# Performance work log

Measured on AMD Instinct MI355X. Metric: run time of the kernel, lower is better.

## Reference

```python
import jax, jax.numpy as jnp
import numpy as np

B, H, W = 32, 56, 56
C_IN, C_OUT, GROUPS, K = 256, 256, 32, 3
EPS = 1e-5


def setup_inputs() -> dict:
    key = jax.random.key(0)
    k1, k2 = jax.random.split(key, 2)
    x = jax.random.normal(k1, (B, H, W, C_IN), dtype=jnp.float32)
    # HWIO grouped-conv kernel: I = C_IN // GROUPS = 8; equivalent to the
    # concatenation of the 32 per-group [3,3,8,8] Conv2d kernels along O.
    w = jax.random.normal(k2, (K, K, C_IN // GROUPS, C_OUT), dtype=jnp.float32) * 0.05
    b = jnp.zeros((C_OUT,), dtype=jnp.float32)
    gamma = jnp.ones((C_OUT,), dtype=jnp.float32)
    beta = jnp.zeros((C_OUT,), dtype=jnp.float32)
    return {"x": x, "w": w, "b": b, "gamma": gamma, "beta": beta}


def reference(x, w, b, gamma, beta):
    # Grouped conv: same math as tf.split -> per-group Conv2d -> tf.concat,
    # expressed as one native grouped convolution (feature_group_count).
    y = jax.lax.conv_general_dilated(
        x, w,
        window_strides=(1, 1),
        padding="SAME",
        dimension_numbers=("NHWC", "HWIO", "NHWC"),
        feature_group_count=GROUPS,
    ) + b  # [B,H,W,C_OUT]
    # BatchNorm (training forward: batch statistics over N,H,W per channel)
    mean = jnp.mean(y, axis=(0, 1, 2))
    var = jnp.var(y, axis=(0, 1, 2))
    y = (y - mean) * jax.lax.rsqrt(var + EPS) * gamma + beta
    # Act('relu')
    return jax.nn.relu(y)
```

## Files before the change

kernel.cpp:

```cpp
#include <hip/hip_runtime.h>
#include <hip/hip_bf16.h>

#define BB 32
#define HH 56
#define WW 56
#define CC 256
#define NPIX (BB*HH*WW)
#define GRP 32
#define GSZ (NPIX*8)
#define EPS 1e-5f

typedef short bf16x8 __attribute__((ext_vector_type(8)));
typedef float f32x4  __attribute__((ext_vector_type(4)));

__device__ __forceinline__ unsigned short f2bf(float f) {
    __hip_bfloat16 h = __float2bfloat16(f);
    return *reinterpret_cast<unsigned short*>(&h);
}


__global__ void k0_zero(float* stats) { stats[threadIdx.x] = 0.f; }

__global__ __launch_bounds__(256) void k_pre(
    const float* __restrict__ x, __hip_bfloat16* __restrict__ xg)
{
    __shared__ unsigned short lx[32*260];
    const int t  = threadIdx.x;
    const int P0 = blockIdx.x * 32;

    #pragma unroll
    for (int r = 0; r < 8; ++r) {
        const int id  = r*256 + t;
        const int pix = id >> 6;
        const int c4  = id & 63;
        float4 v = *(const float4*)(x + (size_t)(P0+pix)*CC + c4*4);
        ushort4 s;
        s.x = f2bf(v.x); s.y = f2bf(v.y); s.z = f2bf(v.z); s.w = f2bf(v.w);
        *(ushort4*)(lx + pix*260 + c4*4) = s;
    }
    __syncthreads();
    #pragma unroll
    for (int r = 0; r < 4; ++r) {
        const int oid = r*256 + t;
        const int pl  = oid & 31;
        const int g   = oid >> 5;
        ushort4 a = *(const ushort4*)(lx + pl*260 + g*8);
        ushort4 c = *(const ushort4*)(lx + pl*260 + g*8 + 4);
        __hip_bfloat16* dst = xg + (size_t)g*GSZ + (size_t)(P0+pl)*8;
        *(ushort4*)dst       = a;
        *(ushort4*)(dst + 4) = c;
    }
}

__global__ __launch_bounds__(256, 5) void k1_conv(
    const __hip_bfloat16* __restrict__ xg, const float* __restrict__ wgt,
    __hip_bfloat16* __restrict__ y, float* __restrict__ stats)
{
    __shared__ unsigned short xt[10*58*24];
    __shared__ float bsum[16], bsq[16];

    const int gp = blockIdx.x;
    const int hb = blockIdx.y;
    const int b  = blockIdx.z;
    const int t  = threadIdx.x;
    const int h0 = hb * 8;

    if (t < 16) { bsum[t] = 0.f; bsq[t] = 0.f; }

    #pragma unroll
    for (int j = 0; j < 5; ++j) {
        const int e   = j*256 + t;
        const int col = e % 58;
        const int rg  = e / 58;
        const int row = rg >> 1;
        const int g   = rg & 1;
        const int hh  = h0 - 1 + row;
        const int wc  = col - 1;
        uint4 v = make_uint4(0u, 0u, 0u, 0u);
        if (e < 1160 && (unsigned)hh < HH && (unsigned)wc < WW)
            v = *(const uint4*)(xg + (size_t)(gp*2+g)*GSZ
                                   + (size_t)((b*HH + hh)*WW + wc)*8);
        if (e < 1160)
            *(uint4*)(xt + (row*58 + col)*24 + g*8) = v;
    }

    const int lane = t & 63;
    const int rp   = t >> 6;
    const int n    = lane & 15;
    const int q    = lane >> 4;

    bf16x8 wfrag[5];
    #pragma unroll
    for (int s = 0; s < 5; ++s) {
        const int o   = s*4 + q;
        const int g   = (o >= 10);
        const int tap = o - g*10;
        bf16x8 f = {0,0,0,0,0,0,0,0};
        if (tap < 9 && (n >> 3) == g) {
            #pragma unroll
            for (int e = 0; e < 8; ++e)
                f[e] = (short)f2bf(wgt[(tap*8 + e)*CC + gp*16 + n]);
        }
        wfrag[s] = f;
    }

    __syncthreads();

    const int m    = lane & 15;
    const int rowr = rp*2 + (m >> 3);
    const int colb = m & 7;

    int aoff[5];
    #pragma unroll
    for (int s = 0; s < 5; ++s) {
        int o  = s*4 + q;
        int g  = (o >= 10);
        int tp = o - g*10;
        if (tp == 9) tp = 0;
        int dh = tp / 3, dw = tp - dh*3;
        aoff[s] = ((rowr + dh)*58 + colb + dw)*24 + g*8;
    }

    const int h = h0 + rowr;
    const size_t pixbase = ((size_t)(b*HH + h))*WW;
    float lsum[4] = {0.f, 0.f, 0.f, 0.f};
    float lsq[4]  = {0.f, 0.f, 0.f, 0.f};

    #pragma unroll 2
    for (int ct = 0; ct < 7; ++ct) {
        f32x4 acc = {0.f, 0.f, 0.f, 0.f};
        #pragma unroll
        for (int s = 0; s < 5; ++s) {
            bf16x8 af = *(const bf16x8*)(xt + aoff[s] + ct*192);
            acc = __builtin_amdgcn_mfma_f32_16x16x32_bf16(wfrag[s], af, acc, 0, 0, 0);
        }
        ushort4 st;
        st.x = f2bf(acc[0]); st.y = f2bf(acc[1]);
        st.z = f2bf(acc[2]); st.w = f2bf(acc[3]);
        *(ushort4*)(y + (pixbase + ct*8 + colb)*CC + gp*16 + q*4) = st;
        #pragma unroll
        for (int i = 0; i < 4; ++i) {
            lsum[i] += acc[i];
            lsq[i]  += acc[i]*acc[i];
        }
    }

    #pragma unroll
    for (int d = 8; d >= 1; d >>= 1) {
        #pragma unroll
        for (int i = 0; i < 4; ++i) {
            lsum[i] += __shfl_xor(lsum[i], d);
            lsq[i]  += __shfl_xor(lsq[i],  d);
        }
    }
    if (m == 0) {
        #pragma unroll
        for (int i = 0; i < 4; ++i) {
            atomicAdd(&bsum[q*4 + i], lsum[i]);
            atomicAdd(&bsq[q*4 + i],  lsq[i]);
        }
    }
    __syncthreads();
    if (t < 16) {
        atomicAdd(&stats[gp*16 + t],       bsum[t]);
        atomicAdd(&stats[256 + gp*16 + t], bsq[t]);
    }
}

__global__ void k2_finalize(const float* __restrict__ stats,
                            const float* __restrict__ gamma,
                            const float* __restrict__ beta,
                            float* __restrict__ ss)
{
    int c = threadIdx.x;
    float inv_n = 1.f / (float)NPIX;
    float mean = stats[c] * inv_n;
    float var  = stats[256 + c] * inv_n - mean * mean;
    float scale = gamma[c] * rsqrtf(var + EPS);
    ss[c]       = scale;
    ss[256 + c] = beta[c] - mean * scale;
}

__global__ __launch_bounds__(256) void k3_norm(
    const __hip_bfloat16* __restrict__ y, const float* __restrict__ ss,
    float* __restrict__ out)
{
    const int t   = threadIdx.x;
    const int oct = t & 31;
    const int pr  = t >> 5;
    const int c0  = oct * 8;

    float4 sc0 = *(const float4*)(ss + c0);
    float4 sc1 = *(const float4*)(ss + c0 + 4);
    float4 sh0 = *(const float4*)(ss + 256 + c0);
    float4 sh1 = *(const float4*)(ss + 256 + c0 + 4);

    const uint4* yv = (const uint4*)y;
    float4* ov = (float4*)out;
    const int px0 = blockIdx.x * 32 + pr;

    uint4 d[4];
    #pragma unroll
    for (int i = 0; i < 4; ++i)
        d[i] = yv[(size_t)(px0 + i*8)*32 + oct];

    #pragma unroll
    for (int i = 0; i < 4; ++i) {
        const int px = px0 + i*8;
        float f0 = __uint_as_float((d[i].x & 0xffffu) << 16);
        float f1 = __uint_as_float(d[i].x & 0xffff0000u);
        float f2 = __uint_as_float((d[i].y & 0xffffu) << 16);
        float f3 = __uint_as_float(d[i].y & 0xffff0000u);
        float f4 = __uint_as_float((d[i].z & 0xffffu) << 16);
        float f5 = __uint_as_float(d[i].z & 0xffff0000u);
        float f6 = __uint_as_float((d[i].w & 0xffffu) << 16);
        float f7 = __uint_as_float(d[i].w & 0xffff0000u);

        float4 o0, o1;
        o0.x = fmaxf(0.f, f0 * sc0.x + sh0.x);
        o0.y = fmaxf(0.f, f1 * sc0.y + sh0.y);
        o0.z = fmaxf(0.f, f2 * sc0.z + sh0.z);
        o0.w = fmaxf(0.f, f3 * sc0.w + sh0.w);
        o1.x = fmaxf(0.f, f4 * sc1.x + sh1.x);
        o1.y = fmaxf(0.f, f5 * sc1.y + sh1.y);
        o1.z = fmaxf(0.f, f6 * sc1.z + sh1.z);
        o1.w = fmaxf(0.f, f7 * sc1.w + sh1.w);

        ov[(size_t)px*64 + oct*2]     = o0;
        ov[(size_t)px*64 + oct*2 + 1] = o1;
    }
}

extern "C" void kernel_launch(void* const* d_in, const int* in_sizes, int n_in,
                              void* d_out, int out_size, void* d_ws, size_t ws_size,
                              hipStream_t stream) {
    const float* x     = (const float*)d_in[0];
    const float* wgt   = (const float*)d_in[1];
    const float* gamma = (const float*)d_in[3];
    const float* beta  = (const float*)d_in[4];
    float* out = (float*)d_out;

    float* stats = (float*)d_ws;
    float* ss    = (float*)((char*)d_ws + 2048);
    __hip_bfloat16* y  = (__hip_bfloat16*)((char*)d_ws + 4096);
    __hip_bfloat16* xg = (__hip_bfloat16*)((char*)d_ws + 4096 + (size_t)NPIX*CC*2);

    k0_zero<<<1, 512, 0, stream>>>(stats);
    k_pre<<<NPIX/32, 256, 0, stream>>>(x, xg);
    k1_conv<<<dim3(16, 7, BB), 256, 0, stream>>>(xg, wgt, y, stats);
    k2_finalize<<<1, 256, 0, stream>>>(stats, gamma, beta, ss);
    k3_norm<<<NPIX/32, 256, 0, stream>>>(y, ss, out);
}
```

Before: 253.3 us.

## Store conv output group-planar, fold stat zeroing and BN finalize into other kernels

```diff
diff --git a/kernel.cpp b/kernel.cpp
--- a/kernel.cpp
+++ b/kernel.cpp
@@ -19,14 +19,17 @@
 }
 
 
-__global__ void k0_zero(float* stats) { stats[threadIdx.x] = 0.f; }
-
 __global__ __launch_bounds__(256) void k_pre(
-    const float* __restrict__ x, __hip_bfloat16* __restrict__ xg)
+    const float* __restrict__ x, __hip_bfloat16* __restrict__ xg,
+    float* __restrict__ stats)
 {
     __shared__ unsigned short lx[32*260];
     const int t  = threadIdx.x;
     const int P0 = blockIdx.x * 32;
+
+    if (blockIdx.x == 0 && t < 128) {
+        *(float4*)(stats + t*4) = make_float4(0.f, 0.f, 0.f, 0.f);
+    }
 
     #pragma unroll
     for (int r = 0; r < 8; ++r) {
@@ -54,7 +57,7 @@
 
 __global__ __launch_bounds__(256, 5) void k1_conv(
     const __hip_bfloat16* __restrict__ xg, const float* __restrict__ wgt,
-    __hip_bfloat16* __restrict__ y, float* __restrict__ stats)
+    __hip_bfloat16* __restrict__ yg, float* __restrict__ stats)
 {
     __shared__ unsigned short xt[10*58*24];
     __shared__ float bsum[16], bsq[16];
@@ -137,7 +140,7 @@
         ushort4 st;
         st.x = f2bf(acc[0]); st.y = f2bf(acc[1]);
         st.z = f2bf(acc[2]); st.w = f2bf(acc[3]);
-        *(ushort4*)(y + (pixbase + ct*8 + colb)*CC + gp*16 + q*4) = st;
+        *(ushort4*)(yg + ((size_t)gp*NPIX + pixbase + ct*8 + colb)*16 + q*4) = st;
         #pragma unroll
         for (int i = 0; i < 4; ++i) {
             lsum[i] += acc[i];
@@ -167,67 +170,69 @@
     }
 }
 
-__global__ void k2_finalize(const float* __restrict__ stats,
-                            const float* __restrict__ gamma,
-                            const float* __restrict__ beta,
-                            float* __restrict__ ss)
-{
-    int c = threadIdx.x;
-    float inv_n = 1.f / (float)NPIX;
-    float mean = stats[c] * inv_n;
-    float var  = stats[256 + c] * inv_n - mean * mean;
-    float scale = gamma[c] * rsqrtf(var + EPS);
-    ss[c]       = scale;
-    ss[256 + c] = beta[c] - mean * scale;
-}
-
 __global__ __launch_bounds__(256) void k3_norm(
-    const __hip_bfloat16* __restrict__ y, const float* __restrict__ ss,
+    const __hip_bfloat16* __restrict__ yg, const float* __restrict__ stats,
+    const float* __restrict__ gamma, const float* __restrict__ beta,
     float* __restrict__ out)
 {
-    const int t   = threadIdx.x;
+    __shared__ unsigned short lx[32*260];
+    const int t  = threadIdx.x;
+    const int P0 = blockIdx.x * 32;
+
+    #pragma unroll
+    for (int r = 0; r < 2; ++r) {
+        const int id = r*256 + t;
+        const int g  = id >> 5;
+        const int pl = id & 31;
+        const __hip_bfloat16* src = yg + ((size_t)g*NPIX + P0 + pl)*16;
+        uint4 v0 = *(const uint4*)(src);
+        uint4 v1 = *(const uint4*)(src + 8);
+        *(uint4*)(lx + pl*260 + g*16)     = v0;
+        *(uint4*)(lx + pl*260 + g*16 + 8) = v1;
+    }
+
     const int oct = t & 31;
     const int pr  = t >> 5;
     const int c0  = oct * 8;
-
-    float4 sc0 = *(const float4*)(ss + c0);
-    float4 sc1 = *(const float4*)(ss + c0 + 4);
-    float4 sh0 = *(const float4*)(ss + 256 + c0);
-    float4 sh1 = *(const float4*)(ss + 256 + c0 + 4);
-
-    const uint4* yv = (const uint4*)y;
-    float4* ov = (float4*)out;
-    const int px0 = blockIdx.x * 32 + pr;
-
-    uint4 d[4];
-    #pragma unroll
-    for (int i = 0; i < 4; ++i)
-        d[i] = yv[(size_t)(px0 + i*8)*32 + oct];
+    const float inv_n = 1.f / (float)NPIX;
+    float sc[8], sh[8];
+    #pragma unroll
+    for (int i = 0; i < 8; ++i) {
+        float mean = stats[c0+i] * inv_n;
+        float var  = stats[256+c0+i] * inv_n - mean*mean;
+        float s    = gamma[c0+i] * rsqrtf(var + EPS);
+        sc[i] = s;
+        sh[i] = beta[c0+i] - mean * s;
+    }
+    __syncthreads();
 
     #pragma unroll
     for (int i = 0; i < 4; ++i) {
-        const int px = px0 + i*8;
-        float f0 = __uint_as_float((d[i].x & 0xffffu) << 16);
-        float f1 = __uint_as_float(d[i].x & 0xffff0000u);
-        float f2 = __uint_as_float((d[i].y & 0xffffu) << 16);
-        float f3 = __uint_as_float(d[i].y & 0xffff0000u);
-        float f4 = __uint_as_float((d[i].z & 0xffffu) << 16);
-        float f5 = __uint_as_float(d[i].z & 0xffff0000u);
-        float f6 = __uint_as_float((d[i].w & 0xffffu) << 16);
-        float f7 = __uint_as_float(d[i].w & 0xffff0000u);
+        const int pl = pr + i*8;
+        ushort4 a = *(const ushort4*)(lx + pl*260 + c0);
+        ushort4 c = *(const ushort4*)(lx + pl*260 + c0 + 4);
+        float f0 = __uint_as_float((unsigned)a.x << 16);
+        float f1 = __uint_as_float((unsigned)a.y << 16);
+        float f2 = __uint_as_float((unsigned)a.z << 16);
+        float f3 = __uint_as_float((unsigned)a.w << 16);
+        float f4 = __uint_as_float((unsigned)c.x << 16);
+        float f5 = __uint_as_float((unsigned)c.y << 16);
+        float f6 = __uint_as_float((unsigned)c.z << 16);
+        float f7 = __uint_as_float((unsigned)c.w << 16);
 
         float4 o0, o1;
-        o0.x = fmaxf(0.f, f0 * sc0.x + sh0.x);
-        o0.y = fmaxf(0.f, f1 * sc0.y + sh0.y);
-        o0.z = fmaxf(0.f, f2 * sc0.z + sh0.z);
-        o0.w = fmaxf(0.f, f3 * sc0.w + sh0.w);
-        o1.x = fmaxf(0.f, f4 * sc1.x + sh1.x);
-        o1.y = fmaxf(0.f, f5 * sc1.y + sh1.y);
-        o1.z = fmaxf(0.f, f6 * sc1.z + sh1.z);
-        o1.w = fmaxf(0.f, f7 * sc1.w + sh1.w);
-
-        ov[(size_t)px*64 + oct*2]     = o0;
-        ov[(size_t)px*64 + oct*2 + 1] = o1;
+        o0.x = fmaxf(0.f, f0 * sc[0] + sh[0]);
+        o0.y = fmaxf(0.f, f1 * sc[1] + sh[1]);
+        o0.z = fmaxf(0.f, f2 * sc[2] + sh[2]);
+        o0.w = fmaxf(0.f, f3 * sc[3] + sh[3]);
+        o1.x = fmaxf(0.f, f4 * sc[4] + sh[4]);
+        o1.y = fmaxf(0.f, f5 * sc[5] + sh[5]);
+        o1.z = fmaxf(0.f, f6 * sc[6] + sh[6]);
+        o1.w = fmaxf(0.f, f7 * sc[7] + sh[7]);
+
+        float* dst = out + (size_t)(P0 + pl)*CC + c0;
+        *(float4*)(dst)     = o0;
+        *(float4*)(dst + 4) = o1;
     }
 }
 
@@ -241,13 +246,10 @@
     float* out = (float*)d_out;
 
     float* stats = (float*)d_ws;
-    float* ss    = (float*)((char*)d_ws + 2048);
-    __hip_bfloat16* y  = (__hip_bfloat16*)((char*)d_ws + 4096);
+    __hip_bfloat16* yg = (__hip_bfloat16*)((char*)d_ws + 4096);
     __hip_bfloat16* xg = (__hip_bfloat16*)((char*)d_ws + 4096 + (size_t)NPIX*CC*2);
 
-    k0_zero<<<1, 512, 0, stream>>>(stats);
-    k_pre<<<NPIX/32, 256, 0, stream>>>(x, xg);
-    k1_conv<<<dim3(16, 7, BB), 256, 0, stream>>>(xg, wgt, y, stats);
-    k2_finalize<<<1, 256, 0, stream>>>(stats, gamma, beta, ss);
-    k3_norm<<<NPIX/32, 256, 0, stream>>>(y, ss, out);
-}
+    k_pre<<<NPIX/32, 256, 0, stream>>>(x, xg, stats);
+    k1_conv<<<dim3(16, 7, BB), 256, 0, stream>>>(xg, wgt, yg, stats);
+    k3_norm<<<NPIX/32, 256, 0, stream>>>(yg, stats, gamma, beta, out);
+}
```

New measurement: 236.9 us. 6.5% less time.
